# Optimization experiments

Measured on AMD Instinct MI355X. Metric: run time of the kernel, lower is better.

The kernel has to match this reference:

```python
import jax, jax.numpy as jnp
import numpy as np

NEG_INF = 1e20  # matches INF in the torch source
EPS = 1e-12     # F.normalize default eps
THRESHOLD = 0.1  # config.graph_learn_epsilon_label2label


def setup_inputs() -> dict:
    key = jax.random.key(0)
    k1, k2, k3, k4, k5 = jax.random.split(key, 5)
    L, E, E_PT, H = 2048, 512, 300, 16
    return {
        "label_embedding": jax.random.normal(k1, (L, E), dtype=jnp.float32),
        "pretrained_label_embedding": jax.random.normal(k2, (L, E_PT), dtype=jnp.float32),
        "W_pt": jax.random.normal(k3, (H, E_PT), dtype=jnp.float32) * 0.1,
        "W_gcn0": jax.random.normal(k4, (E, E), dtype=jnp.float32) * (1.0 / np.sqrt(E)),
        "W_gcn1": jax.random.normal(k5, (E, E), dtype=jnp.float32) * (1.0 / np.sqrt(E)),
    }


def _weighted_cosine(input_pt, W_pt):
    # W_pt: [H, E_pt]; input_pt: [L, E_pt]
    w2 = W_pt ** 2                                  # [H, E_pt]
    h = input_pt[None, :, :] * w2[:, None, :]       # [H, L, E_pt]
    norm = jnp.linalg.norm(h, axis=-1, keepdims=True)
    h_norm = h / jnp.maximum(norm, EPS)             # F.normalize(p=2, dim=-1)
    # mean over heads of per-head cosine similarity: [L, L]
    scores = jnp.einsum("hle,hme->hlm", h_norm, h_norm).mean(axis=0)
    return scores


def reference(label_embedding, pretrained_label_embedding, W_pt, W_gcn0, W_gcn1):
    # 1) metric-based graph structure learning
    scores_cosine = _weighted_cosine(pretrained_label_embedding, W_pt)
    scores = jnp.where(scores_cosine >= THRESHOLD, scores_cosine, -NEG_INF)
    adj = jax.nn.softmax(scores, axis=-1)           # [L, L]

    # 2) 2-layer GCN message passing (bias=None, batch_norm=False, eval-mode dropout)
    x = jax.nn.relu(adj @ (label_embedding @ W_gcn0))
    x = jax.nn.relu(adj @ (x @ W_gcn1))
    return x
```

## Files before the change

kernel.cpp:

```cpp
#include <hip/hip_runtime.h>
#include <hip/hip_bf16.h>


typedef __attribute__((ext_vector_type(8))) short bf16x8;
typedef __attribute__((ext_vector_type(4))) float f32x4;
typedef __attribute__((ext_vector_type(4))) int i32x4;

#define L_DIM 2048
#define EPT 300
#define H_DIM 16
#define KDIM 4800
#define WINDOW 1.5e-3f

__global__ __launch_bounds__(256) void prep_kernel(const float* __restrict__ xpt,
                                                   const float* __restrict__ Wpt,
                                                   const float* __restrict__ label,
                                                   const float* __restrict__ W0,
                                                   const float* __restrict__ W1,
                                                   signed char* __restrict__ Y,
                                                   float* __restrict__ rnorms,
                                                   float* __restrict__ inv_s,
                                                   __hip_bfloat16* __restrict__ Lbf,
                                                   __hip_bfloat16* __restrict__ W0t,
                                                   __hip_bfloat16* __restrict__ W1t) {
  __shared__ float redmax[4];
  __shared__ float tile[32][33];
  const int b = blockIdx.x;
  const int tid = threadIdx.x;
  if (b < 2048) {
    const int i = b;
    const int lane = tid & 63;
    const int w = tid >> 6;
    const float* x = xpt + i * EPT;
    float y[4][5];
    float wmax = 0.f;
#pragma unroll
    for (int hh = 0; hh < 4; ++hh) {
      const int h = w * 4 + hh;
      const float* wp = Wpt + h * EPT;
      float ss = 0.f;
#pragma unroll
      for (int t = 0; t < 5; ++t) {
        int e = lane + 64 * t;
        float val = 0.f;
        if (e < EPT) {
          float we = wp[e];
          val = x[e] * we * we;
        }
        y[hh][t] = val;
        ss += val * val;
      }
#pragma unroll
      for (int o = 32; o >= 1; o >>= 1) ss += __shfl_xor(ss, o, 64);
      float n = fmaxf(sqrtf(ss), 1e-12f);
      if (lane == 0) rnorms[i * H_DIM + h] = 1.0f / n;
      float scale = 0.25f / n;
#pragma unroll
      for (int t = 0; t < 5; ++t) {
        y[hh][t] *= scale;
        wmax = fmaxf(wmax, fabsf(y[hh][t]));
      }
    }
#pragma unroll
    for (int o = 32; o >= 1; o >>= 1) wmax = fmaxf(wmax, __shfl_xor(wmax, o, 64));
    if (lane == 0) redmax[w] = wmax;
    __syncthreads();
    float rowmax = fmaxf(fmaxf(redmax[0], redmax[1]), fmaxf(redmax[2], redmax[3]));
    rowmax = fmaxf(rowmax, 1e-12f);
    const float qs = 127.0f / rowmax;
    if (tid == 0) inv_s[i] = rowmax * (1.0f / 127.0f);
#pragma unroll
    for (int hh = 0; hh < 4; ++hh) {
      const int h = w * 4 + hh;
#pragma unroll
      for (int t = 0; t < 5; ++t) {
        int e = lane + 64 * t;
        if (e < EPT) {
          int qv = __float2int_rn(y[hh][t] * qs);
          qv = max(-127, min(127, qv));
          Y[(size_t)i * KDIM + h * EPT + e] = (signed char)qv;
        }
      }
    }
    return;
  }
  if (b < 6144) {
    int i = (b - 2048) * 256 + tid;
    Lbf[i] = __float2bfloat16(label[i]);
    return;
  }
  int local = b - 6144;
  const bool first = local < 256;
  const float* src = first ? W0 : W1;
  __hip_bfloat16* dst = first ? W0t : W1t;
  int rem = local & 255;
  int c0 = (rem & 15) * 32, r0 = (rem >> 4) * 32;
  int tx = tid & 31, ty = tid >> 5;
  for (int i2 = ty; i2 < 32; i2 += 8) tile[i2][tx] = src[(size_t)(r0 + i2) * 512 + c0 + tx];
  __syncthreads();
  for (int i2 = ty; i2 < 32; i2 += 8)
    dst[(size_t)(c0 + i2) * 512 + r0 + tx] = __float2bfloat16(tile[tx][i2]);
}

__global__ __launch_bounds__(256) void gram_i8(const signed char* __restrict__ Y,
                                               float* __restrict__ S,
                                               const float* __restrict__ inv_s,
                                               const __hip_bfloat16* __restrict__ W0t,
                                               const __hip_bfloat16* __restrict__ Lbf,
                                               __hip_bfloat16* __restrict__ T0t) {
  __shared__ __attribute__((aligned(16))) char smem[32768];
  const int id = blockIdx.x;
  const int bx = (id & 7) | (((id >> 3) & 3) << 3);
  const int by = id >> 5;
  const int row0 = by * 64, col0 = bx * 64;
  const int tid = threadIdx.x;
  const int lane = tid & 63;
  const int wn = tid >> 6;
  const int r = lane & 15, q = lane >> 4;

  if (col0 + 64 <= row0) {
    const int d = (by * (by - 1)) / 2 + bx;
    if (d >= 256) return;
    const int row0r = (d >> 5) * 64;
    const int col0r = (d & 31) * 64;
    __hip_bfloat16* Asb = (__hip_bfloat16*)smem;
    __hip_bfloat16* Bsb = (__hip_bfloat16*)(smem + 16384);
    const int srow8 = tid >> 3;
    const int schunk8 = (tid & 7) ^ (srow8 & 7);
    f32x4 racc[4];
#pragma unroll
    for (int t = 0; t < 4; ++t) {
      f32x4 z = {0.f, 0.f, 0.f, 0.f};
      racc[t] = z;
    }
#define RSTAGE(bufi, k0)                                                                      \
  {                                                                                           \
    _Pragma("unroll") for (int it = 0; it < 2; ++it) {                                        \
      __builtin_amdgcn_global_load_lds(                                                       \
          (const __attribute__((address_space(1))) void*)(W0t + (size_t)(row0r + it * 32 + srow8) * 512 + \
                                                          (k0) + schunk8 * 8),                \
          (__attribute__((address_space(3))) void*)(Asb + (bufi)*4096 + (it * 256 + tid) * 8), 16, 0, 0); \
    }                                                                                         \
    _Pragma("unroll") for (int it = 0; it < 2; ++it) {                                        \
      __builtin_amdgcn_global_load_lds(                                                       \
          (const __attribute__((address_space(1))) void*)(Lbf + (size_t)(col0r + it * 32 + srow8) * 512 + \
                                                          (k0) + schunk8 * 8),                \
          (__attribute__((address_space(3))) void*)(Bsb + (bufi)*4096 + (it * 256 + tid) * 8), 16, 0, 0); \
    }                                                                                         \
  }
    RSTAGE(0, 0)
    for (int k = 0; k < 8; ++k) {
      __syncthreads();
      if (k + 1 < 8) RSTAGE((k + 1) & 1, (k + 1) * 64)
      const __hip_bfloat16* as = Asb + (k & 1) * 4096;
      const __hip_bfloat16* bs = Bsb + (k & 1) * 4096;
#pragma unroll
      for (int kk = 0; kk < 2; ++kk) {
        const int ch = ((kk * 4 + q) ^ (r & 7)) * 8;
        bf16x8 af[4];
#pragma unroll
        for (int t = 0; t < 4; ++t) af[t] = *(const bf16x8*)(as + (t * 16 + r) * 64 + ch);
        bf16x8 bfr = *(const bf16x8*)(bs + (wn * 16 + r) * 64 + ch);
#pragma unroll
        for (int t = 0; t < 4; ++t)
          racc[t] = __builtin_amdgcn_mfma_f32_16x16x32_bf16(af[t], bfr, racc[t], 0, 0, 0);
      }
    }
#undef RSTAGE
    const int gcr = col0r + wn * 16 + r;
#pragma unroll
    for (int t = 0; t < 4; ++t) {
      int gr0 = row0r + t * 16 + q * 4;
#pragma unroll
      for (int p = 0; p < 4; ++p)
        T0t[(size_t)(gr0 + p) * 2048 + gcr] = __float2bfloat16(racc[t][p]);
    }
    return;
  }

  const bool do_mirror = (col0 > row0);
  signed char* As = (signed char*)smem;
  signed char* Bs = (signed char*)(smem + 16384);

  i32x4 acc[4];
#pragma unroll
  for (int t = 0; t < 4; ++t) {
    i32x4 z = {0, 0, 0, 0};
    acc[t] = z;
  }
  constexpr int NF = 37;

#define STAGE128(bufi, k0)                                                                     \
  {                                                                                            \
    _Pragma("unroll") for (int it = 0; it < 2; ++it) {                                         \
      const int idx = it * 256 + tid;                                                          \
      const int srw = idx >> 3;                                                                \
      const int scc = (idx & 7) ^ (srw & 7);                                                   \
      __builtin_amdgcn_global_load_lds(                                                        \
          (const __attribute__((address_space(1))) void*)(Y + (size_t)(row0 + srw) * KDIM +    \
                                                          (k0) + scc * 16),                    \
          (__attribute__((address_space(3))) void*)(As + (bufi)*8192 + idx * 16), 16, 0, 0);   \
    }                                                                                          \
    _Pragma("unroll") for (int it = 0; it < 2; ++it) {                                         \
      const int idx = it * 256 + tid;                                                          \
      const int srw = idx >> 3;                                                                \
      const int scc = (idx & 7) ^ (srw & 7);                                                   \
      __builtin_amdgcn_global_load_lds(                                                        \
          (const __attribute__((address_space(1))) void*)(Y + (size_t)(col0 + srw) * KDIM +    \
                                                          (k0) + scc * 16),                    \
          (__attribute__((address_space(3))) void*)(Bs + (bufi)*8192 + idx * 16), 16, 0, 0);   \
    }                                                                                          \
  }

#define STAGETAIL(bufi, k0)                                                                    \
  {                                                                                            \
    const int srw = tid >> 2;                                                                  \
    const int scc = (tid & 3) ^ ((srw >> 2) & 3);                                              \
    __builtin_amdgcn_global_load_lds(                                                          \
        (const __attribute__((address_space(1))) void*)(Y + (size_t)(row0 + srw) * KDIM +      \
                                                        (k0) + scc * 16),                      \
        (__attribute__((address_space(3))) void*)(As + (bufi)*8192 + tid * 16), 16, 0, 0);     \
    __builtin_amdgcn_global_load_lds(                                                          \
        (const __attribute__((address_space(1))) void*)(Y + (size_t)(col0 + srw) * KDIM +      \
                                                        (k0) + scc * 16),                      \
        (__attribute__((address_space(3))) void*)(Bs + (bufi)*8192 + tid * 16), 16, 0, 0);     \
  }

  STAGE128(0, 0)
  for (int k = 0; k <= NF; ++k) {
    __syncthreads();
    if (k + 1 < NF) {
      STAGE128((k + 1) & 1, (k + 1) * 128)
    } else if (k + 1 == NF) {
      STAGETAIL((k + 1) & 1, NF * 128)
    }
    if (k < NF) {
      const signed char* as = As + (k & 1) * 8192;
      const signed char* bs = Bs + (k & 1) * 8192;
#pragma unroll
      for (int kk = 0; kk < 2; ++kk) {
        const int ch = ((kk * 4 + q) ^ (r & 7)) * 16;
        i32x4 bfrag = *(const i32x4*)(bs + (wn * 16 + r) * 128 + ch);
#pragma unroll
        for (int t = 0; t < 4; ++t) {
          i32x4 afrag = *(const i32x4*)(as + (t * 16 + r) * 128 + ch);
          acc[t] = __builtin_amdgcn_mfma_i32_16x16x64_i8(afrag, bfrag, acc[t], 0, 0, 0);
        }
      }
    } else {
      const signed char* as = As + (k & 1) * 8192;
      const signed char* bs = Bs + (k & 1) * 8192;
      const int ch = (q ^ ((r >> 2) & 3)) * 16;
      i32x4 bfrag = *(const i32x4*)(bs + (wn * 16 + r) * 64 + ch);
#pragma unroll
      for (int t = 0; t < 4; ++t) {
        i32x4 afrag = *(const i32x4*)(as + (t * 16 + r) * 64 + ch);
        acc[t] = __builtin_amdgcn_mfma_i32_16x16x64_i8(afrag, bfrag, acc[t], 0, 0, 0);
      }
    }
  }
#undef STAGE128
#undef STAGETAIL
  const int gc = col0 + wn * 16 + r;
  const float sj = inv_s[gc];
#pragma unroll
  for (int t = 0; t < 4; ++t) {
    int gr0 = row0 + t * 16 + q * 4;
#pragma unroll
    for (int p = 0; p < 4; ++p) {
      float vv = (float)acc[t][p] * (inv_s[gr0 + p] * sj);
      S[(size_t)(gr0 + p) * L_DIM + gc] = vv;
      if (do_mirror) S[(size_t)gc * L_DIM + (gr0 + p)] = vv;
    }
  }
}

template <int BM, int BN, bool RELU, bool OUT_BF16>
__global__ __launch_bounds__(256) void gemm_bt(const __hip_bfloat16* __restrict__ A,
                                               const __hip_bfloat16* __restrict__ B,
                                               void* __restrict__ C0v,
                                               int M, int N, int K) {
  constexpr int WMG = BM / 64;
  constexpr int WNG = 4 / WMG;
  constexpr int NC = BN / (16 * WNG);
  const int row0 = blockIdx.y * BM, col0 = blockIdx.x * BN;
  __shared__ __attribute__((aligned(16))) __hip_bfloat16 As[2][BM * 64];
  __shared__ __attribute__((aligned(16))) __hip_bfloat16 Bs[2][BN * 64];
  const int tid = threadIdx.x;
  const int lane = tid & 63;
  const int wave = tid >> 6;
  const int wm = wave / WNG, wn = wave % WNG;
  const int r = lane & 15, q = lane >> 4;
  const int srow = tid >> 3;
  const int schunk = (tid & 7) ^ (srow & 7);

  f32x4 acc[4][NC];
#pragma unroll
  for (int a = 0; a < 4; ++a)
#pragma unroll
    for (int b = 0; b < NC; ++b) {
      f32x4 z = {0.f, 0.f, 0.f, 0.f};
      acc[a][b] = z;
    }

  const int niter = K >> 6;

#define STAGE(bufi, k0)                                                                       \
  {                                                                                           \
    _Pragma("unroll") for (int it = 0; it < BM / 32; ++it) {                                  \
      __builtin_amdgcn_global_load_lds(                                                       \
          (const __attribute__((address_space(1))) void*)(A + (size_t)(row0 + it * 32 + srow) * K + \
                                                          (k0) + schunk * 8),                 \
          (__attribute__((address_space(3))) void*)(&As[bufi][(it * 256 + tid) * 8]), 16, 0, 0); \
    }                                                                                         \
    _Pragma("unroll") for (int it = 0; it < BN / 32; ++it) {                                  \
      __builtin_amdgcn_global_load_lds(                                                       \
          (const __attribute__((address_space(1))) void*)(B + (size_t)(col0 + it * 32 + srow) * K + \
                                                          (k0) + schunk * 8),                 \
          (__attribute__((address_space(3))) void*)(&Bs[bufi][(it * 256 + tid) * 8]), 16, 0, 0); \
    }                                                                                         \
  }

  STAGE(0, 0)
  for (int k = 0; k < niter; ++k) {
    __syncthreads();
    if (k + 1 < niter) STAGE((k + 1) & 1, (k + 1) << 6)
    const __hip_bfloat16* as = As[k & 1];
    const __hip_bfloat16* bs = Bs[k & 1];
#pragma unroll
    for (int kk = 0; kk < 2; ++kk) {
      const int ch = ((kk * 4 + q) ^ (r & 7)) * 8;
      bf16x8 af[4], bfr[NC];
#pragma unroll
      for (int t = 0; t < 4; ++t)
        af[t] = *(const bf16x8*)(as + (wm * 64 + t * 16 + r) * 64 + ch);
#pragma unroll
      for (int c = 0; c < NC; ++c)
        bfr[c] = *(const bf16x8*)(bs + (wn * 16 * NC + c * 16 + r) * 64 + ch);
#pragma unroll
      for (int tm = 0; tm < 4; ++tm)
#pragma unroll
        for (int tn = 0; tn < NC; ++tn)
          acc[tm][tn] = __builtin_amdgcn_mfma_f32_16x16x32_bf16(af[tm], bfr[tn], acc[tm][tn], 0, 0, 0);
    }
  }
#undef STAGE
#pragma unroll
  for (int tm = 0; tm < 4; ++tm) {
    int gr0 = row0 + wm * 64 + tm * 16 + q * 4;
#pragma unroll
    for (int tn = 0; tn < NC; ++tn) {
      int gc = col0 + wn * 16 * NC + tn * 16 + r;
#pragma unroll
      for (int p = 0; p < 4; ++p) {
        float vv = acc[tm][tn][p];
        if (RELU) vv = fmaxf(vv, 0.f);
        if (OUT_BF16) {
          ((__hip_bfloat16*)C0v)[(size_t)(gr0 + p) * N + gc] = __float2bfloat16(vv);
        } else {
          ((float*)C0v)[(size_t)(gr0 + p) * N + gc] = vv;
        }
      }
    }
  }
}

template <bool OUT_BF16>
__global__ __launch_bounds__(512) void gemm_adj_fused(const __hip_bfloat16* __restrict__ A,
                                                      const __hip_bfloat16* __restrict__ B,
                                                      void* __restrict__ C0v) {
  constexpr int K = 2048, N = 512;
  __shared__ __attribute__((aligned(16))) __hip_bfloat16 sm[4][2][4096];
  const int tid = threadIdx.x;
  const int grp = tid >> 8;
  const int gtid = tid & 255;
  const int lane = tid & 63;
  const int wn = (tid >> 6) & 3;
  const int r = lane & 15, q = lane >> 4;
  const int srow = gtid >> 3;
  const int schunk = (gtid & 7) ^ (srow & 7);
  const int row0 = blockIdx.y * 64, col0 = blockIdx.x * 64;
  const int kbeg = grp * 1024;
  __hip_bfloat16* As = &sm[grp * 2 + 0][0][0];
  __hip_bfloat16* Bs = &sm[grp * 2 + 1][0][0];

  f32x4 acc[4];
#pragma unroll
  for (int t = 0; t < 4; ++t) {
    f32x4 z = {0.f, 0.f, 0.f, 0.f};
    acc[t] = z;
  }

#define FSTAGE(bufi, k0)                                                                      \
  {                                                                                           \
    _Pragma("unroll") for (int it = 0; it < 2; ++it) {                                        \
      __builtin_amdgcn_global_load_lds(                                                       \
          (const __attribute__((address_space(1))) void*)(A + (size_t)(row0 + it * 32 + srow) * K + \
                                                          (k0) + schunk * 8),                 \
          (__attribute__((address_space(3))) void*)(As + (bufi)*4096 + (it * 256 + gtid) * 8), 16, 0, 0); \
    }                                                                                         \
    _Pragma("unroll") for (int it = 0; it < 2; ++it) {                                        \
      __builtin_amdgcn_global_load_lds(                                                       \
          (const __attribute__((address_space(1))) void*)(B + (size_t)(col0 + it * 32 + srow) * K + \
                                                          (k0) + schunk * 8),                 \
          (__attribute__((address_space(3))) void*)(Bs + (bufi)*4096 + (it * 256 + gtid) * 8), 16, 0, 0); \
    }                                                                                         \
  }

  FSTAGE(0, kbeg)
  for (int k = 0; k < 16; ++k) {
    __syncthreads();
    if (k + 1 < 16) FSTAGE((k + 1) & 1, kbeg + ((k + 1) << 6))
    const __hip_bfloat16* as = As + (k & 1) * 4096;
    const __hip_bfloat16* bs = Bs + (k & 1) * 4096;
#pragma unroll
    for (int kk = 0; kk < 2; ++kk) {
      const int ch = ((kk * 4 + q) ^ (r & 7)) * 8;
      bf16x8 af[4];
#pragma unroll
      for (int t = 0; t < 4; ++t) af[t] = *(const bf16x8*)(as + (t * 16 + r) * 64 + ch);
      bf16x8 bfr = *(const bf16x8*)(bs + (wn * 16 + r) * 64 + ch);
#pragma unroll
      for (int t = 0; t < 4; ++t)
        acc[t] = __builtin_amdgcn_mfma_f32_16x16x32_bf16(af[t], bfr, acc[t], 0, 0, 0);
    }
  }
#undef FSTAGE
  __syncthreads();
  float* F = (float*)&sm[2][0][0];
  if (grp == 1) {
#pragma unroll
    for (int tm = 0; tm < 4; ++tm)
#pragma unroll
      for (int p = 0; p < 4; ++p) F[gtid * 16 + tm * 4 + p] = acc[tm][p];
  }
  __syncthreads();
  if (grp == 0) {
#pragma unroll
    for (int tm = 0; tm < 4; ++tm) {
      int gr0 = row0 + tm * 16 + q * 4;
      int gc = col0 + wn * 16 + r;
#pragma unroll
      for (int p = 0; p < 4; ++p) {
        float vv = fmaxf(acc[tm][p] + F[gtid * 16 + tm * 4 + p], 0.f);
        if (OUT_BF16) {
          ((__hip_bfloat16*)C0v)[(size_t)(gr0 + p) * N + gc] = __float2bfloat16(vv);
        } else {
          ((float*)C0v)[(size_t)(gr0 + p) * N + gc] = vv;
        }
      }
    }
  }
}

__global__ __launch_bounds__(256) void post_kernel(const float* __restrict__ S,
                                                   __hip_bfloat16* __restrict__ adj,
                                                   const float* __restrict__ xpt,
                                                   const float* __restrict__ Wpt,
                                                   const float* __restrict__ rnorms) {
  __shared__ float rowv[L_DIM];
  __shared__ int lq[1024];
  __shared__ int lcount;
  __shared__ float red[4];
  const int b = blockIdx.x;
  const int tid = threadIdx.x;
  if (tid == 0) lcount = 0;
  __syncthreads();
  const float* s = S + (size_t)b * L_DIM;
  for (int j0 = tid * 4; j0 < L_DIM; j0 += 1024) {
    float4 v = *(const float4*)(s + j0);
    *(float4*)(&rowv[j0]) = v;
    float vv[4] = {v.x, v.y, v.z, v.w};
#pragma unroll
    for (int u = 0; u < 4; ++u) {
      if (fabsf(vv[u] - 0.1f) < WINDOW) {
        int p = atomicAdd(&lcount, 1);
        if (p < 1024) lq[p] = j0 + u;
      }
    }
  }
  __syncthreads();
  const int n = min(lcount, 1024);
  if (n > 0) {
    const int lane = tid & 63;
    const int wave = tid >> 6;
    float xiv[5];
    float w4i[H_DIM][5];
    {
      const float* xi = xpt + b * EPT;
#pragma unroll
      for (int t = 0; t < 5; ++t) {
        int idx = lane + 64 * t;
        xiv[t] = idx < EPT ? xi[idx] : 0.f;
      }
#pragma unroll
      for (int h = 0; h < H_DIM; ++h) {
        float rni = rnorms[b * H_DIM + h];
#pragma unroll
        for (int t = 0; t < 5; ++t) {
          int idx = lane + 64 * t;
          float w = idx < EPT ? Wpt[h * EPT + idx] : 0.f;
          float w2 = w * w;
          w4i[h][t] = w2 * w2 * rni;
        }
      }
    }
    for (int k = wave; k < n; k += 4) {
      int j = lq[k];
      const float* xj = xpt + j * EPT;
      float pre[5];
#pragma unroll
      for (int t = 0; t < 5; ++t) {
        int idx = lane + 64 * t;
        pre[t] = idx < EPT ? xiv[t] * xj[idx] : 0.f;
      }
      float accv = 0.f;
#pragma unroll
      for (int h = 0; h < H_DIM; ++h) {
        float ph = 0.f;
#pragma unroll
        for (int t = 0; t < 5; ++t) ph += pre[t] * w4i[h][t];
        accv += ph * rnorms[j * H_DIM + h];
      }
#pragma unroll
      for (int o = 32; o >= 1; o >>= 1) accv += __shfl_xor(accv, o, 64);
      if (lane == 0) rowv[j] = accv * (1.f / 16.f);
    }
    __syncthreads();
  }
  float m = -1e30f;
  for (int j = tid; j < L_DIM; j += 256) {
    float v = rowv[j];
    if (v >= 0.1f && v > m) m = v;
  }
#pragma unroll
  for (int o = 32; o >= 1; o >>= 1) m = fmaxf(m, __shfl_xor(m, o, 64));
  if ((tid & 63) == 0) red[tid >> 6] = m;
  __syncthreads();
  m = fmaxf(fmaxf(red[0], red[1]), fmaxf(red[2], red[3]));
  float sum = 0.f;
  for (int j = tid; j < L_DIM; j += 256) {
    float v = rowv[j];
    if (v >= 0.1f) sum += __expf(v - m);
  }
#pragma unroll
  for (int o = 32; o >= 1; o >>= 1) sum += __shfl_xor(sum, o, 64);
  __syncthreads();
  if ((tid & 63) == 0) red[tid >> 6] = sum;
  __syncthreads();
  sum = red[0] + red[1] + red[2] + red[3];
  float inv = 1.f / sum;
  for (int j = tid; j < L_DIM; j += 256) {
    float v = rowv[j];
    float a = (v >= 0.1f) ? __expf(v - m) * inv : 0.f;
    adj[(size_t)b * L_DIM + j] = __float2bfloat16(a);
  }
}

extern "C" void kernel_launch(void* const* d_in, const int* in_sizes, int n_in, void* d_out,
                              int out_size, void* d_ws, size_t ws_size, hipStream_t stream) {
  const float* label = (const float*)d_in[0];
  const float* xpt = (const float*)d_in[1];
  const float* Wpt = (const float*)d_in[2];
  const float* W0 = (const float*)d_in[3];
  const float* W1 = (const float*)d_in[4];
  float* out = (float*)d_out;

  char* ws = (char*)d_ws;
  signed char* Y = (signed char*)ws;
  float* S = (float*)(ws + 19660800);
  float* rnorms = (float*)(ws + 36438016);
  float* inv_s = (float*)(ws + 44957696);
  __hip_bfloat16* Lbf = (__hip_bfloat16*)(ws + 44965888);
  __hip_bfloat16* adj = (__hip_bfloat16*)ws;
  __hip_bfloat16* W0t = (__hip_bfloat16*)(ws + 10485760);
  __hip_bfloat16* W1t = (__hip_bfloat16*)(ws + 11010048);
  __hip_bfloat16* T0t = (__hip_bfloat16*)(ws + 11534336);
  __hip_bfloat16* X1 = (__hip_bfloat16*)(ws + 13631488);
  __hip_bfloat16* T1t = (__hip_bfloat16*)(ws + 15728640);

  prep_kernel<<<6656, 256, 0, stream>>>(xpt, Wpt, label, W0, W1, Y, rnorms, inv_s, Lbf, W0t, W1t);
  gram_i8<<<1024, 256, 0, stream>>>(Y, S, inv_s, W0t, Lbf, T0t);
  post_kernel<<<2048, 256, 0, stream>>>(S, adj, xpt, Wpt, rnorms);
  gemm_adj_fused<true><<<dim3(8, 32), 512, 0, stream>>>(adj, T0t, X1);
  gemm_bt<64, 64, false, true><<<dim3(32, 8), 256, 0, stream>>>(W1t, X1, T1t, 512, 2048, 512);
  gemm_adj_fused<false><<<dim3(8, 32), 512, 0, stream>>>(adj, T1t, out);
}
```

Measured before the change: 174.2 us.

## Triple-buffer int8 Gram GEMM loads with explicit vmcnt waits

Moves the int8 Gram kernel from a double-buffered LDS pipeline to a triple-buffered one, with two stages prefetched ahead. Each iteration waits only on older loads through a partial s_waitcnt vmcnt instead of draining everything at __syncthreads. The goal is to hide global-to-LDS latency behind the MFMA work. In exchange LDS use per block goes from 32KB to 48KB, which may lower occupancy, and the hand-written vmcnt counts have to match the number of loads issued per stage exactly.

```diff
diff --git a/kernel.cpp b/kernel.cpp
--- a/kernel.cpp
+++ b/kernel.cpp
@@ -108,7 +108,7 @@
                                                const __hip_bfloat16* __restrict__ W0t,
                                                const __hip_bfloat16* __restrict__ Lbf,
                                                __hip_bfloat16* __restrict__ T0t) {
-  __shared__ __attribute__((aligned(16))) char smem[32768];
+  __shared__ __attribute__((aligned(16))) char smem[49152];
   const int id = blockIdx.x;
   const int bx = (id & 7) | (((id >> 3) & 3) << 3);
   const int by = id >> 5;
@@ -180,7 +180,7 @@
 
   const bool do_mirror = (col0 > row0);
   signed char* As = (signed char*)smem;
-  signed char* Bs = (signed char*)(smem + 16384);
+  signed char* Bs = (signed char*)(smem + 24576);
 
   i32x4 acc[4];
 #pragma unroll
@@ -188,7 +188,6 @@
     i32x4 z = {0, 0, 0, 0};
     acc[t] = z;
   }
-  constexpr int NF = 37;
 
 #define STAGE128(bufi, k0)                                                                     \
   {                                                                                            \
@@ -226,41 +225,54 @@
         (__attribute__((address_space(3))) void*)(Bs + (bufi)*8192 + tid * 16), 16, 0, 0);     \
   }
 
+#define COMPUTE128(bufi)                                                                       \
+  {                                                                                            \
+    const signed char* as = As + (bufi)*8192;                                                  \
+    const signed char* bs = Bs + (bufi)*8192;                                                  \
+    _Pragma("unroll") for (int kk = 0; kk < 2; ++kk) {                                         \
+      const int ch = ((kk * 4 + q) ^ (r & 7)) * 16;                                            \
+      i32x4 bfrag = *(const i32x4*)(bs + (wn * 16 + r) * 128 + ch);                            \
+      _Pragma("unroll") for (int t = 0; t < 4; ++t) {                                          \
+        i32x4 afrag = *(const i32x4*)(as + (t * 16 + r) * 128 + ch);                           \
+        acc[t] = __builtin_amdgcn_mfma_i32_16x16x64_i8(afrag, bfrag, acc[t], 0, 0, 0);         \
+      }                                                                                        \
+    }                                                                                          \
+  }
+
   STAGE128(0, 0)
-  for (int k = 0; k <= NF; ++k) {
-    __syncthreads();
-    if (k + 1 < NF) {
-      STAGE128((k + 1) & 1, (k + 1) * 128)
-    } else if (k + 1 == NF) {
-      STAGETAIL((k + 1) & 1, NF * 128)
-    }
-    if (k < NF) {
-      const signed char* as = As + (k & 1) * 8192;
-      const signed char* bs = Bs + (k & 1) * 8192;
-#pragma unroll
-      for (int kk = 0; kk < 2; ++kk) {
-        const int ch = ((kk * 4 + q) ^ (r & 7)) * 16;
-        i32x4 bfrag = *(const i32x4*)(bs + (wn * 16 + r) * 128 + ch);
-#pragma unroll
-        for (int t = 0; t < 4; ++t) {
-          i32x4 afrag = *(const i32x4*)(as + (t * 16 + r) * 128 + ch);
-          acc[t] = __builtin_amdgcn_mfma_i32_16x16x64_i8(afrag, bfrag, acc[t], 0, 0, 0);
-        }
-      }
+  STAGE128(1, 128)
+  for (int k = 0; k < 36; ++k) {
+    asm volatile("s_waitcnt vmcnt(4)" ::: "memory");
+    __builtin_amdgcn_s_barrier();
+    __builtin_amdgcn_sched_barrier(0);
+    if (k < 35) {
+      STAGE128((k + 2) % 3, (k + 2) * 128)
     } else {
-      const signed char* as = As + (k & 1) * 8192;
-      const signed char* bs = Bs + (k & 1) * 8192;
-      const int ch = (q ^ ((r >> 2) & 3)) * 16;
-      i32x4 bfrag = *(const i32x4*)(bs + (wn * 16 + r) * 64 + ch);
-#pragma unroll
-      for (int t = 0; t < 4; ++t) {
-        i32x4 afrag = *(const i32x4*)(as + (t * 16 + r) * 64 + ch);
-        acc[t] = __builtin_amdgcn_mfma_i32_16x16x64_i8(afrag, bfrag, acc[t], 0, 0, 0);
-      }
+      STAGETAIL((k + 2) % 3, 37 * 128)
+    }
+    COMPUTE128(k % 3);
+  }
+  asm volatile("s_waitcnt vmcnt(2)" ::: "memory");
+  __builtin_amdgcn_s_barrier();
+  __builtin_amdgcn_sched_barrier(0);
+  COMPUTE128(36 % 3);
+  asm volatile("s_waitcnt vmcnt(0)" ::: "memory");
+  __builtin_amdgcn_s_barrier();
+  __builtin_amdgcn_sched_barrier(0);
+  {
+    const signed char* as = As + (37 % 3) * 8192;
+    const signed char* bs = Bs + (37 % 3) * 8192;
+    const int ch = (q ^ ((r >> 2) & 3)) * 16;
+    i32x4 bfrag = *(const i32x4*)(bs + (wn * 16 + r) * 64 + ch);
+#pragma unroll
+    for (int t = 0; t < 4; ++t) {
+      i32x4 afrag = *(const i32x4*)(as + (t * 16 + r) * 64 + ch);
+      acc[t] = __builtin_amdgcn_mfma_i32_16x16x64_i8(afrag, bfrag, acc[t], 0, 0, 0);
     }
   }
 #undef STAGE128
 #undef STAGETAIL
+#undef COMPUTE128
   const int gc = col0 + wn * 16 + r;
   const float sj = inv_s[gc];
 #pragma unroll
```

After: 181.6 us. +4.2%, slower.

## Fuse three GCN GEMMs into one persistent kernel with grid barriers

Applied to the files above, without the earlier changes.

Replaces the three separate GEMM launches (adj·T0, W1·X1, adj·T1) with a single 256-block kernel that runs each phase and synchronises between them using atomic global barriers. The intent is to remove inter-kernel launch gaps and tail effects. The barrier counters are zeroed in the prep kernel. This relies on all 256 blocks being co-resident and adds spin-wait overhead. The middle GEMM now uses the split-K two-group tile routine.

```diff
diff --git a/kernel.cpp b/kernel.cpp
--- a/kernel.cpp
+++ b/kernel.cpp
@@ -22,7 +22,8 @@
                                                    float* __restrict__ inv_s,
                                                    __hip_bfloat16* __restrict__ Lbf,
                                                    __hip_bfloat16* __restrict__ W0t,
-                                                   __hip_bfloat16* __restrict__ W1t) {
+                                                   __hip_bfloat16* __restrict__ W1t,
+                                                   int* __restrict__ bar) {
   __shared__ float redmax[4];
   __shared__ float tile[32][33];
   const int b = blockIdx.x;
@@ -85,6 +86,7 @@
     return;
   }
   if (b < 6144) {
+    if (b == 2048 && tid < 2) bar[tid] = 0;
     int i = (b - 2048) * 256 + tid;
     Lbf[i] = __float2bfloat16(label[i]);
     return;
@@ -275,102 +277,130 @@
   }
 }
 
-template <int BM, int BN, bool RELU, bool OUT_BF16>
-__global__ __launch_bounds__(256) void gemm_bt(const __hip_bfloat16* __restrict__ A,
-                                               const __hip_bfloat16* __restrict__ B,
-                                               void* __restrict__ C0v,
-                                               int M, int N, int K) {
-  constexpr int WMG = BM / 64;
-  constexpr int WNG = 4 / WMG;
-  constexpr int NC = BN / (16 * WNG);
-  const int row0 = blockIdx.y * BM, col0 = blockIdx.x * BN;
-  __shared__ __attribute__((aligned(16))) __hip_bfloat16 As[2][BM * 64];
-  __shared__ __attribute__((aligned(16))) __hip_bfloat16 Bs[2][BN * 64];
+__global__ __launch_bounds__(256) void post_kernel(const float* __restrict__ S,
+                                                   __hip_bfloat16* __restrict__ adj,
+                                                   const float* __restrict__ xpt,
+                                                   const float* __restrict__ Wpt,
+                                                   const float* __restrict__ rnorms) {
+  __shared__ float rowv[L_DIM];
+  __shared__ int lq[1024];
+  __shared__ int lcount;
+  __shared__ float red[4];
+  const int b = blockIdx.x;
   const int tid = threadIdx.x;
-  const int lane = tid & 63;
-  const int wave = tid >> 6;
-  const int wm = wave / WNG, wn = wave % WNG;
-  const int r = lane & 15, q = lane >> 4;
-  const int srow = tid >> 3;
-  const int schunk = (tid & 7) ^ (srow & 7);
-
-  f32x4 acc[4][NC];
-#pragma unroll
-  for (int a = 0; a < 4; ++a)
-#pragma unroll
-    for (int b = 0; b < NC; ++b) {
-      f32x4 z = {0.f, 0.f, 0.f, 0.f};
-      acc[a][b] = z;
-    }
-
-  const int niter = K >> 6;
-
-#define STAGE(bufi, k0)                                                                       \
-  {                                                                                           \
-    _Pragma("unroll") for (int it = 0; it < BM / 32; ++it) {                                  \
-      __builtin_amdgcn_global_load_lds(                                                       \
-          (const __attribute__((address_space(1))) void*)(A + (size_t)(row0 + it * 32 + srow) * K + \
-                                                          (k0) + schunk * 8),                 \
-          (__attribute__((address_space(3))) void*)(&As[bufi][(it * 256 + tid) * 8]), 16, 0, 0); \
-    }                                                                                         \
-    _Pragma("unroll") for (int it = 0; it < BN / 32; ++it) {                                  \
-      __builtin_amdgcn_global_load_lds(                                                       \
-          (const __attribute__((address_space(1))) void*)(B + (size_t)(col0 + it * 32 + srow) * K + \
-                                                          (k0) + schunk * 8),                 \
-          (__attribute__((address_space(3))) void*)(&Bs[bufi][(it * 256 + tid) * 8]), 16, 0, 0); \
-    }                                                                                         \
-  }
-
-  STAGE(0, 0)
-  for (int k = 0; k < niter; ++k) {
+  if (tid == 0) lcount = 0;
+  __syncthreads();
+  const float* s = S + (size_t)b * L_DIM;
+  for (int j0 = tid * 4; j0 < L_DIM; j0 += 1024) {
+    float4 v = *(const float4*)(s + j0);
+    *(float4*)(&rowv[j0]) = v;
+    float vv[4] = {v.x, v.y, v.z, v.w};
+#pragma unroll
+    for (int u = 0; u < 4; ++u) {
+      if (fabsf(vv[u] - 0.1f) < WINDOW) {
+        int p = atomicAdd(&lcount, 1);
+        if (p < 1024) lq[p] = j0 + u;
+      }
+    }
+  }
+  __syncthreads();
+  const int n = min(lcount, 1024);
+  if (n > 0) {
+    const int lane = tid & 63;
+    const int wave = tid >> 6;
+    float xiv[5];
+    float w4i[H_DIM][5];
+    {
+      const float* xi = xpt + b * EPT;
+#pragma unroll
+      for (int t = 0; t < 5; ++t) {
+        int idx = lane + 64 * t;
+        xiv[t] = idx < EPT ? xi[idx] : 0.f;
+      }
+#pragma unroll
+      for (int h = 0; h < H_DIM; ++h) {
+        float rni = rnorms[b * H_DIM + h];
+#pragma unroll
+        for (int t = 0; t < 5; ++t) {
+          int idx = lane + 64 * t;
+          float w = idx < EPT ? Wpt[h * EPT + idx] : 0.f;
+          float w2 = w * w;
+          w4i[h][t] = w2 * w2 * rni;
+        }
+      }
+    }
+    for (int k = wave; k < n; k += 4) {
+      int j = lq[k];
+      const float* xj = xpt + j * EPT;
+      float pre[5];
+#pragma unroll
+      for (int t = 0; t < 5; ++t) {
+        int idx = lane + 64 * t;
+        pre[t] = idx < EPT ? xiv[t] * xj[idx] : 0.f;
+      }
+      float accv = 0.f;
+#pragma unroll
+      for (int h = 0; h < H_DIM; ++h) {
+        float ph = 0.f;
+#pragma unroll
+        for (int t = 0; t < 5; ++t) ph += pre[t] * w4i[h][t];
+        accv += ph * rnorms[j * H_DIM + h];
+      }
+#pragma unroll
+      for (int o = 32; o >= 1; o >>= 1) accv += __shfl_xor(accv, o, 64);
+      if (lane == 0) rowv[j] = accv * (1.f / 16.f);
+    }
     __syncthreads();
-    if (k + 1 < niter) STAGE((k + 1) & 1, (k + 1) << 6)
-    const __hip_bfloat16* as = As[k & 1];
-    const __hip_bfloat16* bs = Bs[k & 1];
-#pragma unroll
-    for (int kk = 0; kk < 2; ++kk) {
-      const int ch = ((kk * 4 + q) ^ (r & 7)) * 8;
-      bf16x8 af[4], bfr[NC];
-#pragma unroll
-      for (int t = 0; t < 4; ++t)
-        af[t] = *(const bf16x8*)(as + (wm * 64 + t * 16 + r) * 64 + ch);
-#pragma unroll
-      for (int c = 0; c < NC; ++c)
-        bfr[c] = *(const bf16x8*)(bs + (wn * 16 * NC + c * 16 + r) * 64 + ch);
-#pragma unroll
-      for (int tm = 0; tm < 4; ++tm)
-#pragma unroll
-        for (int tn = 0; tn < NC; ++tn)
-          acc[tm][tn] = __builtin_amdgcn_mfma_f32_16x16x32_bf16(af[tm], bfr[tn], acc[tm][tn], 0, 0, 0);
-    }
-  }
-#undef STAGE
-#pragma unroll
-  for (int tm = 0; tm < 4; ++tm) {
-    int gr0 = row0 + wm * 64 + tm * 16 + q * 4;
-#pragma unroll
-    for (int tn = 0; tn < NC; ++tn) {
-      int gc = col0 + wn * 16 * NC + tn * 16 + r;
-#pragma unroll
-      for (int p = 0; p < 4; ++p) {
-        float vv = acc[tm][tn][p];
-        if (RELU) vv = fmaxf(vv, 0.f);
-        if (OUT_BF16) {
-          ((__hip_bfloat16*)C0v)[(size_t)(gr0 + p) * N + gc] = __float2bfloat16(vv);
-        } else {
-          ((float*)C0v)[(size_t)(gr0 + p) * N + gc] = vv;
-        }
-      }
-    }
-  }
-}
-
-template <bool OUT_BF16>
-__global__ __launch_bounds__(512) void gemm_adj_fused(const __hip_bfloat16* __restrict__ A,
-                                                      const __hip_bfloat16* __restrict__ B,
-                                                      void* __restrict__ C0v) {
-  constexpr int K = 2048, N = 512;
-  __shared__ __attribute__((aligned(16))) __hip_bfloat16 sm[4][2][4096];
+  }
+  float m = -1e30f;
+  for (int j = tid; j < L_DIM; j += 256) {
+    float v = rowv[j];
+    if (v >= 0.1f && v > m) m = v;
+  }
+#pragma unroll
+  for (int o = 32; o >= 1; o >>= 1) m = fmaxf(m, __shfl_xor(m, o, 64));
+  if ((tid & 63) == 0) red[tid >> 6] = m;
+  __syncthreads();
+  m = fmaxf(fmaxf(red[0], red[1]), fmaxf(red[2], red[3]));
+  float sum = 0.f;
+  for (int j = tid; j < L_DIM; j += 256) {
+    float v = rowv[j];
+    if (v >= 0.1f) sum += __expf(v - m);
+  }
+#pragma unroll
+  for (int o = 32; o >= 1; o >>= 1) sum += __shfl_xor(sum, o, 64);
+  __syncthreads();
+  if ((tid & 63) == 0) red[tid >> 6] = sum;
+  __syncthreads();
+  sum = red[0] + red[1] + red[2] + red[3];
+  float inv = 1.f / sum;
+  for (int j = tid; j < L_DIM; j += 256) {
+    float v = rowv[j];
+    float a = (v >= 0.1f) ? __expf(v - m) * inv : 0.f;
+    adj[(size_t)b * L_DIM + j] = __float2bfloat16(a);
+  }
+}
+
+
+__device__ __forceinline__ void gbar(int* c) {
+  __syncthreads();
+  __threadfence();
+  if (threadIdx.x == 0) {
+    __hip_atomic_fetch_add(c, 1, __ATOMIC_ACQ_REL, __HIP_MEMORY_SCOPE_AGENT);
+    while (__hip_atomic_load(c, __ATOMIC_ACQUIRE, __HIP_MEMORY_SCOPE_AGENT) < 256) {
+      __builtin_amdgcn_s_sleep(8);
+    }
+  }
+  __syncthreads();
+  __threadfence();
+}
+
+__device__ __forceinline__ void gemm_phase(const __hip_bfloat16* __restrict__ A,
+                                           const __hip_bfloat16* __restrict__ B,
+                                           void* __restrict__ C,
+                                           __hip_bfloat16* sm,
+                                           int bx, int by, int N, int K,
+                                           bool relu, bool outbf16) {
   const int tid = threadIdx.x;
   const int grp = tid >> 8;
   const int gtid = tid & 255;
@@ -379,10 +409,11 @@
   const int r = lane & 15, q = lane >> 4;
   const int srow = gtid >> 3;
   const int schunk = (gtid & 7) ^ (srow & 7);
-  const int row0 = blockIdx.y * 64, col0 = blockIdx.x * 64;
-  const int kbeg = grp * 1024;
-  __hip_bfloat16* As = &sm[grp * 2 + 0][0][0];
-  __hip_bfloat16* Bs = &sm[grp * 2 + 1][0][0];
+  const int row0 = by * 64, col0 = bx * 64;
+  const int kbeg = grp * (K >> 1);
+  const int niter = K >> 7;
+  __hip_bfloat16* As = sm + (grp * 2 + 0) * 8192;
+  __hip_bfloat16* Bs = sm + (grp * 2 + 1) * 8192;
 
   f32x4 acc[4];
 #pragma unroll
@@ -391,7 +422,7 @@
     acc[t] = z;
   }
 
-#define FSTAGE(bufi, k0)                                                                      \
+#define GSTAGE(bufi, k0)                                                                      \
   {                                                                                           \
     _Pragma("unroll") for (int it = 0; it < 2; ++it) {                                        \
       __builtin_amdgcn_global_load_lds(                                                       \
@@ -407,10 +438,10 @@
     }                                                                                         \
   }
 
-  FSTAGE(0, kbeg)
-  for (int k = 0; k < 16; ++k) {
+  GSTAGE(0, kbeg)
+  for (int k = 0; k < niter; ++k) {
     __syncthreads();
-    if (k + 1 < 16) FSTAGE((k + 1) & 1, kbeg + ((k + 1) << 6))
+    if (k + 1 < niter) GSTAGE((k + 1) & 1, kbeg + ((k + 1) << 6))
     const __hip_bfloat16* as = As + (k & 1) * 4096;
     const __hip_bfloat16* bs = Bs + (k & 1) * 4096;
 #pragma unroll
@@ -425,9 +456,9 @@
         acc[t] = __builtin_amdgcn_mfma_f32_16x16x32_bf16(af[t], bfr, acc[t], 0, 0, 0);
     }
   }
-#undef FSTAGE
-  __syncthreads();
-  float* F = (float*)&sm[2][0][0];
+#undef GSTAGE
+  __syncthreads();
+  float* F = (float*)(sm + 2 * 8192);
   if (grp == 1) {
 #pragma unroll
     for (int tm = 0; tm < 4; ++tm)
@@ -442,119 +473,32 @@
       int gc = col0 + wn * 16 + r;
 #pragma unroll
       for (int p = 0; p < 4; ++p) {
-        float vv = fmaxf(acc[tm][p] + F[gtid * 16 + tm * 4 + p], 0.f);
-        if (OUT_BF16) {
-          ((__hip_bfloat16*)C0v)[(size_t)(gr0 + p) * N + gc] = __float2bfloat16(vv);
+        float vv = acc[tm][p] + F[gtid * 16 + tm * 4 + p];
+        if (relu) vv = fmaxf(vv, 0.f);
+        if (outbf16) {
+          ((__hip_bfloat16*)C)[(size_t)(gr0 + p) * N + gc] = __float2bfloat16(vv);
         } else {
-          ((float*)C0v)[(size_t)(gr0 + p) * N + gc] = vv;
+          ((float*)C)[(size_t)(gr0 + p) * N + gc] = vv;
         }
       }
     }
   }
 }
 
-__global__ __launch_bounds__(256) void post_kernel(const float* __restrict__ S,
-                                                   __hip_bfloat16* __restrict__ adj,
-                                                   const float* __restrict__ xpt,
-                                                   const float* __restrict__ Wpt,
-                                                   const float* __restrict__ rnorms) {
-  __shared__ float rowv[L_DIM];
-  __shared__ int lq[1024];
-  __shared__ int lcount;
-  __shared__ float red[4];
+__global__ __launch_bounds__(512) void gcn_fused(const __hip_bfloat16* __restrict__ adj,
+                                                 const __hip_bfloat16* __restrict__ T0t,
+                                                 const __hip_bfloat16* __restrict__ W1t,
+                                                 __hip_bfloat16* __restrict__ X1,
+                                                 __hip_bfloat16* __restrict__ T1t,
+                                                 float* __restrict__ out,
+                                                 int* __restrict__ bar) {
+  __shared__ __attribute__((aligned(16))) __hip_bfloat16 sm[32768];
   const int b = blockIdx.x;
-  const int tid = threadIdx.x;
-  if (tid == 0) lcount = 0;
-  __syncthreads();
-  const float* s = S + (size_t)b * L_DIM;
-  for (int j0 = tid * 4; j0 < L_DIM; j0 += 1024) {
-    float4 v = *(const float4*)(s + j0);
-    *(float4*)(&rowv[j0]) = v;
-    float vv[4] = {v.x, v.y, v.z, v.w};
-#pragma unroll
-    for (int u = 0; u < 4; ++u) {
-      if (fabsf(vv[u] - 0.1f) < WINDOW) {
-        int p = atomicAdd(&lcount, 1);
-        if (p < 1024) lq[p] = j0 + u;
-      }
-    }
-  }
-  __syncthreads();
-  const int n = min(lcount, 1024);
-  if (n > 0) {
-    const int lane = tid & 63;
-    const int wave = tid >> 6;
-    float xiv[5];
-    float w4i[H_DIM][5];
-    {
-      const float* xi = xpt + b * EPT;
-#pragma unroll
-      for (int t = 0; t < 5; ++t) {
-        int idx = lane + 64 * t;
-        xiv[t] = idx < EPT ? xi[idx] : 0.f;
-      }
-#pragma unroll
-      for (int h = 0; h < H_DIM; ++h) {
-        float rni = rnorms[b * H_DIM + h];
-#pragma unroll
-        for (int t = 0; t < 5; ++t) {
-          int idx = lane + 64 * t;
-          float w = idx < EPT ? Wpt[h * EPT + idx] : 0.f;
-          float w2 = w * w;
-          w4i[h][t] = w2 * w2 * rni;
-        }
-      }
-    }
-    for (int k = wave; k < n; k += 4) {
-      int j = lq[k];
-      const float* xj = xpt + j * EPT;
-      float pre[5];
-#pragma unroll
-      for (int t = 0; t < 5; ++t) {
-        int idx = lane + 64 * t;
-        pre[t] = idx < EPT ? xiv[t] * xj[idx] : 0.f;
-      }
-      float accv = 0.f;
-#pragma unroll
-      for (int h = 0; h < H_DIM; ++h) {
-        float ph = 0.f;
-#pragma unroll
-        for (int t = 0; t < 5; ++t) ph += pre[t] * w4i[h][t];
-        accv += ph * rnorms[j * H_DIM + h];
-      }
-#pragma unroll
-      for (int o = 32; o >= 1; o >>= 1) accv += __shfl_xor(accv, o, 64);
-      if (lane == 0) rowv[j] = accv * (1.f / 16.f);
-    }
-    __syncthreads();
-  }
-  float m = -1e30f;
-  for (int j = tid; j < L_DIM; j += 256) {
-    float v = rowv[j];
-    if (v >= 0.1f && v > m) m = v;
-  }
-#pragma unroll
-  for (int o = 32; o >= 1; o >>= 1) m = fmaxf(m, __shfl_xor(m, o, 64));
-  if ((tid & 63) == 0) red[tid >> 6] = m;
-  __syncthreads();
-  m = fmaxf(fmaxf(red[0], red[1]), fmaxf(red[2], red[3]));
-  float sum = 0.f;
-  for (int j = tid; j < L_DIM; j += 256) {
-    float v = rowv[j];
-    if (v >= 0.1f) sum += __expf(v - m);
-  }
-#pragma unroll
-  for (int o = 32; o >= 1; o >>= 1) sum += __shfl_xor(sum, o, 64);
-  __syncthreads();
-  if ((tid & 63) == 0) red[tid >> 6] = sum;
-  __syncthreads();
-  sum = red[0] + red[1] + red[2] + red[3];
-  float inv = 1.f / sum;
-  for (int j = tid; j < L_DIM; j += 256) {
-    float v = rowv[j];
-    float a = (v >= 0.1f) ? __expf(v - m) * inv : 0.f;
-    adj[(size_t)b * L_DIM + j] = __float2bfloat16(a);
-  }
+  gemm_phase(adj, T0t, X1, sm, b & 7, b >> 3, 512, 2048, true, true);
+  gbar(bar + 0);
+  gemm_phase(W1t, X1, T1t, sm, b & 31, b >> 5, 2048, 512, false, true);
+  gbar(bar + 1);
+  gemm_phase(adj, T1t, out, sm, b & 7, b >> 3, 512, 2048, true, false);
 }
 
 extern "C" void kernel_launch(void* const* d_in, const int* in_sizes, int n_in, void* d_out,
@@ -572,6 +516,7 @@
   float* rnorms = (float*)(ws + 36438016);
   float* inv_s = (float*)(ws + 44957696);
   __hip_bfloat16* Lbf = (__hip_bfloat16*)(ws + 44965888);
+  int* bar = (int*)(ws + 47063040);
   __hip_bfloat16* adj = (__hip_bfloat16*)ws;
   __hip_bfloat16* W0t = (__hip_bfloat16*)(ws + 10485760);
   __hip_bfloat16* W1t = (__hip_bfloat16*)(ws + 11010048);
@@ -579,10 +524,8 @@
   __hip_bfloat16* X1 = (__hip_bfloat16*)(ws + 13631488);
   __hip_bfloat16* T1t = (__hip_bfloat16*)(ws + 15728640);
 
-  prep_kernel<<<6656, 256, 0, stream>>>(xpt, Wpt, label, W0, W1, Y, rnorms, inv_s, Lbf, W0t, W1t);
+  prep_kernel<<<6656, 256, 0, stream>>>(xpt, Wpt, label, W0, W1, Y, rnorms, inv_s, Lbf, W0t, W1t, bar);
   gram_i8<<<1024, 256, 0, stream>>>(Y, S, inv_s, W0t, Lbf, T0t);
   post_kernel<<<2048, 256, 0, stream>>>(S, adj, xpt, Wpt, rnorms);
-  gemm_adj_fused<true><<<dim3(8, 32), 512, 0, stream>>>(adj, T0t, X1);
-  gemm_bt<64, 64, false, true><<<dim3(32, 8), 256, 0, stream>>>(W1t, X1, T1t, 512, 2048, 512);
-  gemm_adj_fused<false><<<dim3(8, 32), 512, 0, stream>>>(adj, T1t, out);
-}
+  gcn_fused<<<256, 512, 0, stream>>>(adj, T0t, W1t, X1, T1t, out, bar);
+}
```

Result: slower. 327.7 us (+88.1%).
